# Kernel optimization log

Measured on AMD Instinct MI355X. Metric: run time of the kernel, lower is better.

Reference implementation:

```python
import jax, jax.numpy as jnp
import numpy as np

QLEN, MLEN, CMLEN, BSZ, D_MODEL = 1024, 1024, 512, 2, 1024
N_HEAD, D_HEAD, D_INNER = 16, 64, 4096
KLEN = MLEN + CMLEN + QLEN
LN_EPS = 1e-5


def _layer_norm(x, scale, bias):
    mu = jnp.mean(x, axis=-1, keepdims=True)
    var = jnp.var(x, axis=-1, keepdims=True)
    return (x - mu) * jax.lax.rsqrt(var + LN_EPS) * scale + bias


def _rel_shift(x):
    # x: [qlen, klen, bsz, n_head]  (Transformer-XL relative shift)
    q, k, b, n = x.shape
    x = jnp.concatenate([jnp.zeros((q, 1, b, n), x.dtype), x], axis=1)
    x = x.reshape(k + 1, q, b, n)[1:]
    return x.reshape(q, k, b, n)


def setup_inputs() -> dict:
    key = jax.random.key(0)
    ks = jax.random.split(key, 10)
    s = 0.02
    # causal mask: query i (absolute pos MLEN_TOT+i) cannot attend to key j > MLEN_TOT+i
    mlen_tot = KLEN - QLEN
    i = jnp.arange(QLEN)[:, None]
    j = jnp.arange(KLEN)[None, :]
    attn_mask = j > (i + mlen_tot)
    return {
        "input_ids": jax.random.normal(ks[0], (QLEN, BSZ, D_MODEL), jnp.float32),
        "pos_emb": jax.random.normal(ks[1], (KLEN, D_MODEL), jnp.float32),
        "mem": jax.random.normal(ks[2], (MLEN, BSZ, D_MODEL), jnp.float32),
        "c_mem": jax.random.normal(ks[3], (CMLEN, BSZ, D_MODEL), jnp.float32),
        "attn_mask": attn_mask,
        "qkv_w": jax.random.normal(ks[4], (D_MODEL, 3 * N_HEAD * D_HEAD), jnp.float32) * s,
        "r_w": jax.random.normal(ks[5], (D_MODEL, N_HEAD * D_HEAD), jnp.float32) * s,
        "o_w": jax.random.normal(ks[6], (N_HEAD * D_HEAD, D_MODEL), jnp.float32) * s,
        "r_w_bias": jax.random.normal(ks[7], (N_HEAD, D_HEAD), jnp.float32) * s,
        "r_r_bias": jax.random.normal(ks[8], (N_HEAD, D_HEAD), jnp.float32) * s,
        "ln_attn_scale": jnp.ones((D_MODEL,), jnp.float32),
        "ln_attn_bias": jnp.zeros((D_MODEL,), jnp.float32),
        "ff_w1": jax.random.normal(ks[9], (D_MODEL, D_INNER), jnp.float32) * s,
        "ff_b1": jnp.zeros((D_INNER,), jnp.float32),
        "ff_w2": jax.random.normal(jax.random.fold_in(key, 11), (D_INNER, D_MODEL), jnp.float32) * s,
        "ff_b2": jnp.zeros((D_MODEL,), jnp.float32),
        "ln_ff_scale": jnp.ones((D_MODEL,), jnp.float32),
        "ln_ff_bias": jnp.zeros((D_MODEL,), jnp.float32),
    }


def reference(input_ids, pos_emb, mem, c_mem, attn_mask, qkv_w, r_w, o_w,
              r_w_bias, r_r_bias, ln_attn_scale, ln_attn_bias,
              ff_w1, ff_b1, ff_w2, ff_b2, ln_ff_scale, ln_ff_bias):
    qlen, bsz, d_model = input_ids.shape
    n_head, d_head = r_w_bias.shape
    scale = 1.0 / np.sqrt(d_head)

    # _concat_memories + cat with current sequence (seq-first, dim 0)
    mems = jnp.concatenate([mem, c_mem], axis=0)
    cat = jnp.concatenate([mems, input_ids], axis=0)          # [klen, b, d]

    w_heads = cat @ qkv_w                                     # [klen, b, 3*h*dh]
    w_q, w_k, w_v = jnp.split(w_heads, 3, axis=-1)
    w_q = w_q[-qlen:]
    klen = w_k.shape[0]

    w_q = w_q.reshape(qlen, bsz, n_head, d_head)
    w_k = w_k.reshape(klen, bsz, n_head, d_head)
    w_v = w_v.reshape(klen, bsz, n_head, d_head)
    r_k = (pos_emb @ r_w).reshape(klen, n_head, d_head)       # [klen, h, dh]

    AC = jnp.einsum('ibnd,jbnd->ijbn', w_q + r_w_bias, w_k)
    BD = jnp.einsum('ibnd,jnd->ijbn', w_q + r_r_bias, r_k)
    BD = _rel_shift(BD)
    attn_score = (AC + BD) * scale                            # [q, k, b, h]

    attn_score = jnp.where(attn_mask[:, :, None, None], jnp.float32(-1e30), attn_score)
    attn_prob = jax.nn.softmax(attn_score, axis=1)

    attn_vec = jnp.einsum('ijbn,jbnd->ibnd', attn_prob, w_v)
    attn_vec = attn_vec.reshape(qlen, bsz, n_head * d_head)
    attn_out = attn_vec @ o_w

    # post-lnorm residual (pre_lnorm=False)
    attn_res = _layer_norm(input_ids + attn_out, ln_attn_scale, ln_attn_bias)

    # PositionwiseFF (post-lnorm)
    h = jax.nn.relu(attn_res @ ff_w1 + ff_b1) @ ff_w2 + ff_b2
    out = _layer_norm(attn_res + h, ln_ff_scale, ln_ff_bias)
    return out
```

## Files before the change

kernel.cpp:

```cpp
#include <hip/hip_runtime.h>
#include <hip/hip_bf16.h>

#define QLEN 1024
#define KLEN 2560
#define MTOT 1536
#define BSZ 2
#define NH 16
#define DH 64
#define DMODEL 1024
#define DINNER 4096

typedef short bf16x8 __attribute__((ext_vector_type(8)));
typedef float f32x4  __attribute__((ext_vector_type(4)));

__device__ __forceinline__ short f2bf(float f) {
    union { float f; unsigned u; } v; v.f = f;
    unsigned r = v.u + 0x7FFFu + ((v.u >> 16) & 1u);
    return (short)(r >> 16);
}
__device__ __forceinline__ float bf2f(short s) {
    union { unsigned u; float f; } v; v.u = ((unsigned)(unsigned short)s) << 16;
    return v.f;
}
__device__ __forceinline__ unsigned pack2(float a, float b) {
    return (unsigned)(unsigned short)f2bf(a) | ((unsigned)(unsigned short)f2bf(b) << 16);
}

#define GLOAD16(g, l)                                                        \
    __builtin_amdgcn_global_load_lds(                                        \
        (const __attribute__((address_space(1))) unsigned int*)(g),          \
        (__attribute__((address_space(3))) unsigned int*)(l), 16, 0, 0)

__device__ __forceinline__ void tr_body(
    const float* __restrict__ in, short* __restrict__ out,
    int K, int N, int bx, int by, int tid, float (*ts)[65])
{
    const int k0 = by * 64, n0 = bx * 64;
    const int r = tid >> 2, cb = (tid & 3) * 16;
    #pragma unroll
    for (int u = 0; u < 16; u += 4) {
        const float4 v = *(const float4*)(in + (size_t)(k0 + r) * N + n0 + cb + u);
        ts[r][cb + u] = v.x; ts[r][cb + u + 1] = v.y;
        ts[r][cb + u + 2] = v.z; ts[r][cb + u + 3] = v.w;
    }
    __syncthreads();
    #pragma unroll
    for (int p = 0; p < 4; p++) {
        const int wr_ = (tid >> 4) + p * 16;
        const int c   = (tid & 15) * 4;
        uint2 pk;
        pk.x = pack2(ts[c][wr_], ts[c + 1][wr_]);
        pk.y = pack2(ts[c + 2][wr_], ts[c + 3][wr_]);
        *(uint2*)(out + (size_t)(n0 + wr_) * K + k0 + c) = pk;
    }
}

__global__ __launch_bounds__(256) void prep_all(
    const float* __restrict__ mem, const float* __restrict__ cmem,
    const float* __restrict__ inp, short* __restrict__ catb,
    const float* __restrict__ pos, short* __restrict__ posb,
    const float* __restrict__ qkv_w, short* __restrict__ qkv_wt,
    const float* __restrict__ r_w, short* __restrict__ r_wt,
    const float* __restrict__ o_w, short* __restrict__ o_wt,
    const float* __restrict__ ff_w1, short* __restrict__ ff1t,
    const float* __restrict__ ff_w2, short* __restrict__ ff2t)
{
    __shared__ float ts[64][65];
    const int bid = blockIdx.x;
    const int tid = threadIdx.x;
    if (bid < 2560) {
        const int i = bid * 256 + tid;
        const int row = i >> 7, c = (i & 127) * 8;
        const float* src;
        if (row < 2048)      src = mem  + (size_t)row * 1024;
        else if (row < 3072) src = cmem + (size_t)(row - 2048) * 1024;
        else                 src = inp  + (size_t)(row - 3072) * 1024;
        const float4 a = *(const float4*)(src + c);
        const float4 b = *(const float4*)(src + c + 4);
        uint4 o;
        o.x = pack2(a.x, a.y); o.y = pack2(a.z, a.w);
        o.z = pack2(b.x, b.y); o.w = pack2(b.z, b.w);
        *(uint4*)(catb + (size_t)i * 8) = o;
    } else if (bid < 3840) {
        const int i = (bid - 2560) * 256 + tid;
        const float4 a = *(const float4*)(pos + (size_t)i * 8);
        const float4 b = *(const float4*)(pos + (size_t)i * 8 + 4);
        uint4 o;
        o.x = pack2(a.x, a.y); o.y = pack2(a.z, a.w);
        o.z = pack2(b.x, b.y); o.w = pack2(b.z, b.w);
        *(uint4*)(posb + (size_t)i * 8) = o;
    } else if (bid < 4608) {
        const int r = bid - 3840; tr_body(qkv_w, qkv_wt, 1024, 3072, r % 48, r / 48, tid, ts);
    } else if (bid < 4864) {
        const int r = bid - 4608; tr_body(r_w, r_wt, 1024, 1024, r % 16, r / 16, tid, ts);
    } else if (bid < 5120) {
        const int r = bid - 4864; tr_body(o_w, o_wt, 1024, 1024, r % 16, r / 16, tid, ts);
    } else if (bid < 6144) {
        const int r = bid - 5120; tr_body(ff_w1, ff1t, 1024, 4096, r % 64, r / 64, tid, ts);
    } else {
        const int r = bid - 6144; tr_body(ff_w2, ff2t, 4096, 1024, r % 16, r / 16, tid, ts);
    }
}

__global__ __launch_bounds__(256) void vt_conv(
    const short* __restrict__ wh, short* __restrict__ vt)
{
    __shared__ short Ts[64][72];
    const int j0 = blockIdx.x * 64;
    const int bn = blockIdx.y;
    const int b = bn >> 4, n = bn & 15;
    const int tid = threadIdx.x;
    {
        const int key = tid >> 2, c = (tid & 3) * 16;
        const short* p = wh + ((size_t)(j0 + key) * BSZ + b) * 3072 + 2048 + n * 64 + c;
        *(bf16x8*)&Ts[key][c]     = *(const bf16x8*)p;
        *(bf16x8*)&Ts[key][c + 8] = *(const bf16x8*)(p + 8);
    }
    __syncthreads();
    {
        const int d = tid >> 2, kc = (tid & 3) * 16;
        __attribute__((aligned(16))) short tmp[16];
        #pragma unroll
        for (int u = 0; u < 16; u++) tmp[u] = Ts[kc + u][d];
        short* q = vt + ((size_t)(bn * 64) + d) * KLEN + j0 + kc;
        *(uint4*)q       = *(uint4*)tmp;
        *(uint4*)(q + 8) = *((uint4*)tmp + 1);
    }
}

__device__ __forceinline__ void gemm_core(
    const short* __restrict__ A, const short* __restrict__ Bt,
    short* As, short* Bs, int Kfull, int klen, int bm, int bn,
    int tid, f32x4 acc[4][4])
{
    const int w  = tid >> 6;
    const int l  = tid & 63;
    const int lg = l >> 4, lc = l & 15;
    const int wr = w >> 1, wc = w & 1;
    const int srow = 2 * w * 16 + (l >> 2);
    const int scol = (l & 3) * 8;
    const size_t aoff0 = (size_t)(bm + srow) * Kfull + scol;
    const size_t boff0 = (size_t)(bn + srow) * Kfull + scol;
    const size_t rstep = (size_t)16 * Kfull;
    short* lA0 = As + 2 * w * 512;
    short* lA1 = As + (2 * w + 1) * 512;
    short* lB0 = Bs + 2 * w * 512;
    short* lB1 = Bs + (2 * w + 1) * 512;

    for (int k0 = 0; k0 < klen; k0 += 32) {
        GLOAD16(A + aoff0 + k0, lA0);
        GLOAD16(A + aoff0 + rstep + k0, lA1);
        GLOAD16(Bt + boff0 + k0, lB0);
        GLOAD16(Bt + boff0 + rstep + k0, lB1);
        __syncthreads();
        bf16x8 af[4], bfr[4];
        #pragma unroll
        for (int m = 0; m < 4; m++)
            af[m] = *(const bf16x8*)(As + (wr * 64 + m * 16 + lc) * 32 + lg * 8);
        #pragma unroll
        for (int n = 0; n < 4; n++)
            bfr[n] = *(const bf16x8*)(Bs + (wc * 64 + n * 16 + lc) * 32 + lg * 8);
        #pragma unroll
        for (int m = 0; m < 4; m++)
            #pragma unroll
            for (int n = 0; n < 4; n++)
                acc[m][n] = __builtin_amdgcn_mfma_f32_16x16x32_bf16(
                    af[m], bfr[n], acc[m][n], 0, 0, 0);
        __syncthreads();
    }
}

__global__ __launch_bounds__(256) void gemm_g12(
    const short* __restrict__ catb, const short* __restrict__ qkv_wt,
    short* __restrict__ whb,
    const short* __restrict__ posb, const short* __restrict__ r_wt,
    short* __restrict__ rkb)
{
    __shared__ short As[4096], Bs[4096];
    const int tid = threadIdx.x;
    int id = blockIdx.x;
    const short *A, *Bt; short* Cb; int N, bm, bn;
    if (id < 960) { A = catb; Bt = qkv_wt; Cb = whb; N = 3072;
                    bm = (id / 24) * 128; bn = (id % 24) * 128; }
    else { id -= 960; A = posb; Bt = r_wt; Cb = rkb; N = 1024;
           bm = (id / 8) * 128; bn = (id % 8) * 128; }

    f32x4 acc[4][4];
    #pragma unroll
    for (int m = 0; m < 4; m++)
        #pragma unroll
        for (int n = 0; n < 4; n++) acc[m][n] = (f32x4){0.f, 0.f, 0.f, 0.f};
    gemm_core(A, Bt, As, Bs, 1024, 1024, bm, bn, tid, acc);

    const int w = tid >> 6, l = tid & 63, lg = l >> 4, lc = l & 15;
    const int wr = w >> 1, wc = w & 1;
    #pragma unroll
    for (int m = 0; m < 4; m++)
        #pragma unroll
        for (int n = 0; n < 4; n++) {
            const int col = bn + wc * 64 + n * 16 + lc;
            #pragma unroll
            for (int r = 0; r < 4; r++) {
                const int row = bm + wr * 64 + m * 16 + lg * 4 + r;
                Cb[(size_t)row * N + col] = f2bf(acc[m][n][r]);
            }
        }
}

__global__ __launch_bounds__(256) void gemm_relu(
    const short* __restrict__ A, const short* __restrict__ Bt,
    const float* __restrict__ bias, short* __restrict__ Cb,
    int N, int K)
{
    __shared__ short As[4096], Bs[4096];
    const int tid = threadIdx.x;
    const int bm = blockIdx.y * 128, bn = blockIdx.x * 128;
    f32x4 acc[4][4];
    #pragma unroll
    for (int m = 0; m < 4; m++)
        #pragma unroll
        for (int n = 0; n < 4; n++) acc[m][n] = (f32x4){0.f, 0.f, 0.f, 0.f};
    gemm_core(A, Bt, As, Bs, K, K, bm, bn, tid, acc);

    const int w = tid >> 6, l = tid & 63, lg = l >> 4, lc = l & 15;
    const int wr = w >> 1, wc = w & 1;
    #pragma unroll
    for (int m = 0; m < 4; m++)
        #pragma unroll
        for (int n = 0; n < 4; n++) {
            const int col = bn + wc * 64 + n * 16 + lc;
            const float bv = bias[col];
            #pragma unroll
            for (int r = 0; r < 4; r++) {
                const int row = bm + wr * 64 + m * 16 + lg * 4 + r;
                Cb[(size_t)row * N + col] = f2bf(fmaxf(acc[m][n][r] + bv, 0.0f));
            }
        }
}

__global__ __launch_bounds__(256) void gemm_split(
    const short* __restrict__ A, const short* __restrict__ Bt,
    float* __restrict__ C0, float* __restrict__ C1,
    int N, int Kfull, int Ksub)
{
    __shared__ short As[4096], Bs[4096];
    const int tid = threadIdx.x;
    const int z = blockIdx.z;
    const int bm = blockIdx.y * 128, bn = blockIdx.x * 128;
    float* C = z ? C1 : C0;
    f32x4 acc[4][4];
    #pragma unroll
    for (int m = 0; m < 4; m++)
        #pragma unroll
        for (int n = 0; n < 4; n++) acc[m][n] = (f32x4){0.f, 0.f, 0.f, 0.f};
    gemm_core(A + z * Ksub, Bt + z * Ksub, As, Bs, Kfull, Ksub, bm, bn, tid, acc);

    const int w = tid >> 6, l = tid & 63, lg = l >> 4, lc = l & 15;
    const int wr = w >> 1, wc = w & 1;
    #pragma unroll
    for (int m = 0; m < 4; m++)
        #pragma unroll
        for (int n = 0; n < 4; n++) {
            const int col = bn + wc * 64 + n * 16 + lc;
            #pragma unroll
            for (int r = 0; r < 4; r++) {
                const int row = bm + wr * 64 + m * 16 + lg * 4 + r;
                C[(size_t)row * N + col] = acc[m][n][r];
            }
        }
}

__global__ __launch_bounds__(256) void attn_mfma(
    const short* __restrict__ wh,
    const short* __restrict__ vt,
    const short* __restrict__ rk,
    const float* __restrict__ rwb,
    const float* __restrict__ rrb,
    short* __restrict__ po,
    float* __restrict__ ml)
{
    __shared__ __align__(16) short Ks[64 * 64];
    __shared__ __align__(16) short Vs[64 * 64];
    __shared__ __align__(16) short Rs[128 * 64];
    __shared__ __align__(16) short Ps[4][16 * 64];

    const int bid = blockIdx.x;
    const int ib  = (bid >> 3) & 15;
    const int z   = (bid >> 7) & 1;
    const int bn  = ((bid & 7) << 2) | (bid >> 8);
    const int i0  = ib * 64;
    const int b   = bn >> 4, n = bn & 15;
    const int tid = threadIdx.x;
    const int w   = tid >> 6;
    const int l   = tid & 63;
    const int lg  = l >> 4;
    const int lc  = l & 15;
    const int i_base = i0 + 16 * w;

    bf16x8 aqw[2], aqr[2];
    {
        const int i = i_base + lc;
        const short* qp = wh + ((size_t)(MTOT + i) * BSZ + b) * 3072 + n * 64;
        #pragma unroll
        for (int kc = 0; kc < 2; kc++) {
            const bf16x8 q8 = *(const bf16x8*)(qp + kc * 32 + lg * 8);
            const int d0 = kc * 32 + lg * 8;
            #pragma unroll
            for (int e = 0; e < 8; e++) {
                const float qv = bf2f(q8[e]);
                aqw[kc][e] = f2bf(qv + rwb[n * 64 + d0 + e]);
                aqr[kc][e] = f2bf(qv + rrb[n * 64 + d0 + e]);
            }
        }
    }

    f32x4 o_acc[4];
    #pragma unroll
    for (int nt = 0; nt < 4; nt++) o_acc[nt] = (f32x4){0.f, 0.f, 0.f, 0.f};
    float mrun[4]  = {0.f, 0.f, 0.f, 0.f};
    float lpart[4] = {0.f, 0.f, 0.f, 0.f};

    const int jend   = i0 + 1600;
    const int jhalf  = (((jend >> 1) + 63) >> 6) << 6;
    const int jstart = z ? jhalf : 0;
    const int jstop  = z ? jend  : jhalf;

    const int kr0 = (tid * 2) >> 3,     kc0 = (tid * 2) & 7;
    const int kr1 = (tid * 2 + 1) >> 3, kc1 = (tid * 2 + 1) & 7;
    const size_t whK = (size_t)b * 3072 + 1024 + n * 64;
    const size_t vtK = (size_t)(bn * 64) * KLEN;

    bf16x8 pk0, pk1, pv0, pv1;
    pk0 = *(const bf16x8*)(wh + (size_t)(jstart + kr0) * BSZ * 3072 + whK + kc0 * 8);
    pk1 = *(const bf16x8*)(wh + (size_t)(jstart + kr1) * BSZ * 3072 + whK + kc1 * 8);
    pv0 = *(const bf16x8*)(vt + vtK + (size_t)kr0 * KLEN + jstart + kc0 * 8);
    pv1 = *(const bf16x8*)(vt + vtK + (size_t)kr1 * KLEN + jstart + kc1 * 8);

    for (int j0 = jstart; j0 < jstop; j0 += 64) {
        __syncthreads();
        bf16x8 rreg[4];
        const int mbase = j0 - i0 + 960;
        #pragma unroll
        for (int u = 0; u < 4; u++) {
            const int ci  = tid + 256 * u;
            const int row = ci >> 3, c = ci & 7;
            const int m   = mbase + row;
            rreg[u] = (m < KLEN)
                ? *(const bf16x8*)(rk + (size_t)m * 1024 + n * 64 + c * 8)
                : (bf16x8){0, 0, 0, 0, 0, 0, 0, 0};
        }
        *(bf16x8*)(Ks + kr0 * 64 + ((kc0 ^ (kr0 & 7)) * 8)) = pk0;
        *(bf16x8*)(Ks + kr1 * 64 + ((kc1 ^ (kr1 & 7)) * 8)) = pk1;
        *(bf16x8*)(Vs + kr0 * 64 + ((kc0 ^ (kr0 & 7)) * 8)) = pv0;
        *(bf16x8*)(Vs + kr1 * 64 + ((kc1 ^ (kr1 & 7)) * 8)) = pv1;
        #pragma unroll
        for (int u = 0; u < 4; u++) {
            const int ci  = tid + 256 * u;
            const int row = ci >> 3, c = ci & 7;
            *(bf16x8*)(Rs + row * 64 + ((c ^ (row & 7)) * 8)) = rreg[u];
        }
        const int jn = j0 + 64;
        if (jn < jstop) {
            pk0 = *(const bf16x8*)(wh + (size_t)(jn + kr0) * BSZ * 3072 + whK + kc0 * 8);
            pk1 = *(const bf16x8*)(wh + (size_t)(jn + kr1) * BSZ * 3072 + whK + kc1 * 8);
            pv0 = *(const bf16x8*)(vt + vtK + (size_t)kr0 * KLEN + jn + kc0 * 8);
            pv1 = *(const bf16x8*)(vt + vtK + (size_t)kr1 * KLEN + jn + kc1 * 8);
        }
        __syncthreads();

        __builtin_amdgcn_s_setprio(1);
        f32x4 sfr[4];
        #pragma unroll
        for (int jt = 0; jt < 4; jt++) {
            const int row = 16 * jt + lc;
            const int c0 = (lg ^ (row & 7)) * 8, c1 = ((4 + lg) ^ (row & 7)) * 8;
            const bf16x8 bk0 = *(const bf16x8*)(Ks + row * 64 + c0);
            const bf16x8 bk1 = *(const bf16x8*)(Ks + row * 64 + c1);
            f32x4 acc = (f32x4){0.f, 0.f, 0.f, 0.f};
            acc = __builtin_amdgcn_mfma_f32_16x16x32_bf16(aqw[0], bk0, acc, 0, 0, 0);
            acc = __builtin_amdgcn_mfma_f32_16x16x32_bf16(aqw[1], bk1, acc, 0, 0, 0);
            sfr[jt] = acc;
        }
        f32x4 dr[5];
        #pragma unroll
        for (int mt = 0; mt < 5; mt++) {
            const int rrow = 16 * mt + lc + 48 - 16 * w;
            const int c0 = (lg ^ (rrow & 7)) * 8, c1 = ((4 + lg) ^ (rrow & 7)) * 8;
            const bf16x8 br0 = *(const bf16x8*)(Rs + rrow * 64 + c0);
            const bf16x8 br1 = *(const bf16x8*)(Rs + rrow * 64 + c1);
            f32x4 acc = (f32x4){0.f, 0.f, 0.f, 0.f};
            acc = __builtin_amdgcn_mfma_f32_16x16x32_bf16(aqr[0], br0, acc, 0, 0, 0);
            acc = __builtin_amdgcn_mfma_f32_16x16x32_bf16(aqr[1], br1, acc, 0, 0, 0);
            dr[mt] = acc;
        }
        __builtin_amdgcn_s_setprio(0);

        #pragma unroll
        for (int r = 0; r < 4; r++) {
            const int q   = 4 * lg + r;
            const int o   = lc + 15 - q;
            const int src = (l & 48) | (o & 15);
            float sv[4];
            float mx = -1e30f;
            #pragma unroll
            for (int jt = 0; jt < 4; jt++) {
                const float v0 = __shfl(dr[jt][r], src);
                const float v1 = __shfl(dr[jt + 1][r], src);
                const float bd = (o < 16) ? v0 : v1;
                float s = (sfr[jt][r] + bd) * 0.125f;
                if (z) {
                    const int j = j0 + 16 * jt + lc;
                    if (j > i_base + q + MTOT) s = -1e30f;
                }
                sv[jt] = s;
                mx = fmaxf(mx, s);
            }
            if (__any(mx - mrun[r] > 8.0f)) {
                #pragma unroll
                for (int msk = 1; msk <= 8; msk <<= 1)
                    mx = fmaxf(mx, __shfl_xor(mx, msk));
                const float mnew = fmaxf(mrun[r], mx);
                const float corr = __expf(mrun[r] - mnew);
                mrun[r] = mnew;
                lpart[r] *= corr;
                #pragma unroll
                for (int nt = 0; nt < 4; nt++) o_acc[nt][r] *= corr;
            }
            float ps = 0.f;
            #pragma unroll
            for (int jt = 0; jt < 4; jt++) {
                const float p = __expf(sv[jt] - mrun[r]);
                ps += p;
                Ps[w][q * 64 + (((2 * jt + (lc >> 3)) ^ (q & 7)) * 8) + (lc & 7)] = f2bf(p);
            }
            lpart[r] += ps;
        }

        asm volatile("s_waitcnt lgkmcnt(0)" ::: "memory");
        __builtin_amdgcn_sched_barrier(0);

        __builtin_amdgcn_s_setprio(1);
        const int pc0 = (lg ^ (lc & 7)) * 8, pc1 = ((4 + lg) ^ (lc & 7)) * 8;
        const bf16x8 pa0 = *(const bf16x8*)(Ps[w] + lc * 64 + pc0);
        const bf16x8 pa1 = *(const bf16x8*)(Ps[w] + lc * 64 + pc1);
        #pragma unroll
        for (int nt = 0; nt < 4; nt++) {
            const int row = 16 * nt + lc;
            const int c0 = (lg ^ (row & 7)) * 8, c1 = ((4 + lg) ^ (row & 7)) * 8;
            const bf16x8 bv0 = *(const bf16x8*)(Vs + row * 64 + c0);
            const bf16x8 bv1 = *(const bf16x8*)(Vs + row * 64 + c1);
            o_acc[nt] = __builtin_amdgcn_mfma_f32_16x16x32_bf16(pa0, bv0, o_acc[nt], 0, 0, 0);
            o_acc[nt] = __builtin_amdgcn_mfma_f32_16x16x32_bf16(pa1, bv1, o_acc[nt], 0, 0, 0);
        }
        __builtin_amdgcn_s_setprio(0);
    }

    const size_t blk = (size_t)z * 512 + ib * 32 + bn;
    #pragma unroll
    for (int r = 0; r < 4; r++) {
        float lr = lpart[r];
        #pragma unroll
        for (int msk = 1; msk <= 8; msk <<= 1)
            lr += __shfl_xor(lr, msk);
        const int q = 16 * w + 4 * lg + r;
        #pragma unroll
        for (int nt = 0; nt < 4; nt++)
            po[(blk * 64 + q) * 64 + 16 * nt + lc] = f2bf(o_acc[nt][r]);
        if (lc == 0) {
            ml[(blk * 64 + q) * 2 + 0] = mrun[r];
            ml[(blk * 64 + q) * 2 + 1] = lr;
        }
    }
}

__global__ __launch_bounds__(256) void attn_merge(
    const short* __restrict__ po, const float* __restrict__ ml,
    short* __restrict__ av)
{
    const int blk = blockIdx.x;
    const int ib = blk >> 5, bn = blk & 31;
    const int b = bn >> 4, n = bn & 15;
    const int tid = threadIdx.x;
    const int q = tid >> 2, dc = (tid & 3) * 16;
    const size_t r0 = (size_t)blk * 64 + q;
    const size_t r1 = (size_t)(512 + blk) * 64 + q;
    const float m0 = ml[r0 * 2], l0 = ml[r0 * 2 + 1];
    const float m1 = ml[r1 * 2], l1 = ml[r1 * 2 + 1];
    const float M = fmaxf(m0, m1);
    const float c0 = __expf(m0 - M), c1 = __expf(m1 - M);
    const float invL = 1.0f / (l0 * c0 + l1 * c1);
    const bf16x8 a0 = *(const bf16x8*)(po + r0 * 64 + dc);
    const bf16x8 a1 = *(const bf16x8*)(po + r0 * 64 + dc + 8);
    const bf16x8 b0 = *(const bf16x8*)(po + r1 * 64 + dc);
    const bf16x8 b1 = *(const bf16x8*)(po + r1 * 64 + dc + 8);
    __attribute__((aligned(16))) short ov[16];
    #pragma unroll
    for (int e = 0; e < 8; e++) {
        ov[e]     = f2bf((bf2f(a0[e]) * c0 + bf2f(b0[e]) * c1) * invL);
        ov[e + 8] = f2bf((bf2f(a1[e]) * c0 + bf2f(b1[e]) * c1) * invL);
    }
    const int i = ib * 64 + q;
    short* op = av + ((size_t)i * BSZ + b) * 1024 + n * 64 + dc;
    *(uint4*)op       = *(uint4*)ov;
    *(uint4*)(op + 8) = *((uint4*)ov + 1);
}

template <bool WB, bool HASB>
__global__ __launch_bounds__(256) void ln_fuse(
    const float* __restrict__ p0, const float* __restrict__ p1,
    const float* __restrict__ badd, const float* __restrict__ res,
    const float* __restrict__ scale, const float* __restrict__ bias,
    float* __restrict__ out, short* __restrict__ outb)
{
    const int row = blockIdx.x;
    const int tid = threadIdx.x;
    const size_t base = (size_t)row * 1024 + tid * 4;
    const float4 a = *(const float4*)(p0 + base);
    const float4 b = *(const float4*)(p1 + base);
    const float4 rv = *(const float4*)(res + base);
    float v[4] = {a.x + b.x + rv.x, a.y + b.y + rv.y,
                  a.z + b.z + rv.z, a.w + b.w + rv.w};
    if (HASB) {
        const float4 bb = *(const float4*)(badd + tid * 4);
        v[0] += bb.x; v[1] += bb.y; v[2] += bb.z; v[3] += bb.w;
    }
    float s  = v[0] + v[1] + v[2] + v[3];
    float ss = v[0]*v[0] + v[1]*v[1] + v[2]*v[2] + v[3]*v[3];
    #pragma unroll
    for (int off = 32; off >= 1; off >>= 1) {
        s  += __shfl_down(s, off);
        ss += __shfl_down(ss, off);
    }
    __shared__ float red[8];
    const int lane = tid & 63, wid = tid >> 6;
    if (lane == 0) { red[wid] = s; red[4 + wid] = ss; }
    __syncthreads();
    if (tid == 0) {
        red[0] = red[0] + red[1] + red[2] + red[3];
        red[4] = red[4] + red[5] + red[6] + red[7];
    }
    __syncthreads();
    const float mean = red[0] * (1.0f / 1024.0f);
    const float var  = red[4] * (1.0f / 1024.0f) - mean * mean;
    const float rstd = rsqrtf(var + 1e-5f);
    const float4 sc = *(const float4*)(scale + tid * 4);
    const float4 bi = *(const float4*)(bias + tid * 4);
    float4 o;
    o.x = (v[0] - mean) * rstd * sc.x + bi.x;
    o.y = (v[1] - mean) * rstd * sc.y + bi.y;
    o.z = (v[2] - mean) * rstd * sc.z + bi.z;
    o.w = (v[3] - mean) * rstd * sc.w + bi.w;
    *(float4*)(out + base) = o;
    if (WB) {
        uint2 pk;
        pk.x = pack2(o.x, o.y);
        pk.y = pack2(o.z, o.w);
        *(uint2*)(outb + base) = pk;
    }
}

extern "C" void kernel_launch(void* const* d_in, const int* in_sizes, int n_in,
                              void* d_out, int out_size, void* d_ws, size_t ws_size,
                              hipStream_t stream) {
    const float* input_ids = (const float*)d_in[0];
    const float* pos_emb   = (const float*)d_in[1];
    const float* mem       = (const float*)d_in[2];
    const float* c_mem     = (const float*)d_in[3];
    const float* qkv_w     = (const float*)d_in[5];
    const float* r_w       = (const float*)d_in[6];
    const float* o_w       = (const float*)d_in[7];
    const float* r_w_bias  = (const float*)d_in[8];
    const float* r_r_bias  = (const float*)d_in[9];
    const float* ln_a_s    = (const float*)d_in[10];
    const float* ln_a_b    = (const float*)d_in[11];
    const float* ff_w1     = (const float*)d_in[12];
    const float* ff_b1     = (const float*)d_in[13];
    const float* ff_w2     = (const float*)d_in[14];
    const float* ff_b2     = (const float*)d_in[15];
    const float* ln_f_s    = (const float*)d_in[16];
    const float* ln_f_b    = (const float*)d_in[17];

    char* base = (char*)d_ws;
    short* o_wt   = (short*)(base + 0);
    short* ff1t   = (short*)(base + 2097152);
    short* ff2t   = (short*)(base + 10485760);
    short* whb    = (short*)(base + 18874368);
    short* rkb    = (short*)(base + 50331648);
    short* qkv_wt = (short*)(base + 55574528);
    short* catb   = (short*)(base + 61865984);
    short* posb   = (short*)(base + 72351744);
    short* r_wt   = (short*)(base + 77594624);
    short* vtb    = (short*)(base + 55574528);
    short* po     = (short*)(base + 66060288);
    float* mlb    = (float*)(base + 74448896);
    short* avb    = (short*)(base + 74973184);
    float* hp0    = (float*)(base + 18874368);
    float* hp1    = (float*)(base + 27262976);
    float* ares   = (float*)(base + 35651584);
    short* aresb  = (short*)(base + 44040192);
    short* h1b    = (short*)(base + 48234496);

    const dim3 thr(256);

    prep_all<<<dim3(7168), thr, 0, stream>>>(
        mem, c_mem, input_ids, catb, pos_emb, posb,
        qkv_w, qkv_wt, r_w, r_wt, o_w, o_wt, ff_w1, ff1t, ff_w2, ff2t);
    gemm_g12<<<dim3(1120), thr, 0, stream>>>(catb, qkv_wt, whb, posb, r_wt, rkb);
    vt_conv<<<dim3(40, 32), thr, 0, stream>>>(whb, vtb);
    attn_mfma<<<dim3(1024), thr, 0, stream>>>(
        whb, vtb, rkb, r_w_bias, r_r_bias, po, mlb);
    attn_merge<<<dim3(512), thr, 0, stream>>>(po, mlb, avb);
    gemm_split<<<dim3(8, 16, 2), thr, 0, stream>>>(
        avb, o_wt, hp0, hp1, 1024, 1024, 512);
    ln_fuse<true, false><<<dim3(2048), thr, 0, stream>>>(
        hp0, hp1, nullptr, input_ids, ln_a_s, ln_a_b, ares, aresb);
    gemm_relu<<<dim3(32, 16), thr, 0, stream>>>(aresb, ff1t, ff_b1, h1b, 4096, 1024);
    gemm_split<<<dim3(8, 16, 2), thr, 0, stream>>>(
        h1b, ff2t, hp0, hp1, 1024, 4096, 2048);
    ln_fuse<false, true><<<dim3(2048), thr, 0, stream>>>(
        hp0, hp1, ff_b2, ares, ln_f_s, ln_f_b, (float*)d_out, nullptr);
}
```

Before: 295.0 us.

## Widen attention blocks to 128 queries with 8 waves sharing K/V tiles

The attention kernel now uses 512-thread blocks covering 128 query rows instead of 64, so each K, V and positional tile loaded into shared memory serves twice as many queries. Grid size halves, each thread loads one K/V chunk and three R rows, and the R window grows to 192 rows. The merge kernel's indexing is updated to match the new partial-output layout. This cuts global and LDS traffic per query at the cost of fewer blocks, coarser causal-split balance and more shared memory per block.

New measurement: 403.3 us. +36.7%, slower.

```diff
diff --git a/kernel.cpp b/kernel.cpp
--- a/kernel.cpp
+++ b/kernel.cpp
@@ -270,7 +270,7 @@
         }
 }
 
-__global__ __launch_bounds__(256) void attn_mfma(
+__global__ __launch_bounds__(512, 4) void attn_mfma(
     const short* __restrict__ wh,
     const short* __restrict__ vt,
     const short* __restrict__ rk,
@@ -281,14 +281,14 @@
 {
     __shared__ __align__(16) short Ks[64 * 64];
     __shared__ __align__(16) short Vs[64 * 64];
-    __shared__ __align__(16) short Rs[128 * 64];
-    __shared__ __align__(16) short Ps[4][16 * 64];
+    __shared__ __align__(16) short Rs[192 * 64];
+    __shared__ __align__(16) short Ps[8][16 * 64];
 
     const int bid = blockIdx.x;
-    const int ib  = (bid >> 3) & 15;
-    const int z   = (bid >> 7) & 1;
-    const int bn  = ((bid & 7) << 2) | (bid >> 8);
-    const int i0  = ib * 64;
+    const int ibp = (bid >> 3) & 7;
+    const int z   = (bid >> 6) & 1;
+    const int bn  = ((bid & 7) << 2) | (bid >> 7);
+    const int i0  = ibp * 128;
     const int b   = bn >> 4, n = bn & 15;
     const int tid = threadIdx.x;
     const int w   = tid >> 6;
@@ -320,51 +320,41 @@
     float mrun[4]  = {0.f, 0.f, 0.f, 0.f};
     float lpart[4] = {0.f, 0.f, 0.f, 0.f};
 
-    const int jend   = i0 + 1600;
-    const int jhalf  = (((jend >> 1) + 63) >> 6) << 6;
+    const int jend   = i0 + 1664;
+    const int jhalf  = i0 / 2 + 832;
     const int jstart = z ? jhalf : 0;
     const int jstop  = z ? jend  : jhalf;
 
-    const int kr0 = (tid * 2) >> 3,     kc0 = (tid * 2) & 7;
-    const int kr1 = (tid * 2 + 1) >> 3, kc1 = (tid * 2 + 1) & 7;
+    const int kr = tid >> 3, kc = tid & 7;
     const size_t whK = (size_t)b * 3072 + 1024 + n * 64;
     const size_t vtK = (size_t)(bn * 64) * KLEN;
 
-    bf16x8 pk0, pk1, pv0, pv1;
-    pk0 = *(const bf16x8*)(wh + (size_t)(jstart + kr0) * BSZ * 3072 + whK + kc0 * 8);
-    pk1 = *(const bf16x8*)(wh + (size_t)(jstart + kr1) * BSZ * 3072 + whK + kc1 * 8);
-    pv0 = *(const bf16x8*)(vt + vtK + (size_t)kr0 * KLEN + jstart + kc0 * 8);
-    pv1 = *(const bf16x8*)(vt + vtK + (size_t)kr1 * KLEN + jstart + kc1 * 8);
+    bf16x8 pk, pv;
+    pk = *(const bf16x8*)(wh + (size_t)(jstart + kr) * (BSZ * 3072) + whK + kc * 8);
+    pv = *(const bf16x8*)(vt + vtK + (size_t)kr * KLEN + jstart + kc * 8);
 
     for (int j0 = jstart; j0 < jstop; j0 += 64) {
         __syncthreads();
-        bf16x8 rreg[4];
-        const int mbase = j0 - i0 + 960;
-        #pragma unroll
-        for (int u = 0; u < 4; u++) {
-            const int ci  = tid + 256 * u;
-            const int row = ci >> 3, c = ci & 7;
-            const int m   = mbase + row;
+        bf16x8 rreg[3];
+        const int mbase = j0 - i0 + 896;
+        #pragma unroll
+        for (int u = 0; u < 3; u++) {
+            const int m = mbase + kr + 64 * u;
             rreg[u] = (m < KLEN)
-                ? *(const bf16x8*)(rk + (size_t)m * 1024 + n * 64 + c * 8)
+                ? *(const bf16x8*)(rk + (size_t)m * 1024 + n * 64 + kc * 8)
                 : (bf16x8){0, 0, 0, 0, 0, 0, 0, 0};
         }
-        *(bf16x8*)(Ks + kr0 * 64 + ((kc0 ^ (kr0 & 7)) * 8)) = pk0;
-        *(bf16x8*)(Ks + kr1 * 64 + ((kc1 ^ (kr1 & 7)) * 8)) = pk1;
-        *(bf16x8*)(Vs + kr0 * 64 + ((kc0 ^ (kr0 & 7)) * 8)) = pv0;
-        *(bf16x8*)(Vs + kr1 * 64 + ((kc1 ^ (kr1 & 7)) * 8)) = pv1;
-        #pragma unroll
-        for (int u = 0; u < 4; u++) {
-            const int ci  = tid + 256 * u;
-            const int row = ci >> 3, c = ci & 7;
-            *(bf16x8*)(Rs + row * 64 + ((c ^ (row & 7)) * 8)) = rreg[u];
+        *(bf16x8*)(Ks + kr * 64 + ((kc ^ (kr & 7)) * 8)) = pk;
+        *(bf16x8*)(Vs + kr * 64 + ((kc ^ (kr & 7)) * 8)) = pv;
+        #pragma unroll
+        for (int u = 0; u < 3; u++) {
+            const int row = kr + 64 * u;
+            *(bf16x8*)(Rs + row * 64 + ((kc ^ (row & 7)) * 8)) = rreg[u];
         }
         const int jn = j0 + 64;
         if (jn < jstop) {
-            pk0 = *(const bf16x8*)(wh + (size_t)(jn + kr0) * BSZ * 3072 + whK + kc0 * 8);
-            pk1 = *(const bf16x8*)(wh + (size_t)(jn + kr1) * BSZ * 3072 + whK + kc1 * 8);
-            pv0 = *(const bf16x8*)(vt + vtK + (size_t)kr0 * KLEN + jn + kc0 * 8);
-            pv1 = *(const bf16x8*)(vt + vtK + (size_t)kr1 * KLEN + jn + kc1 * 8);
+            pk = *(const bf16x8*)(wh + (size_t)(jn + kr) * (BSZ * 3072) + whK + kc * 8);
+            pv = *(const bf16x8*)(vt + vtK + (size_t)kr * KLEN + jn + kc * 8);
         }
         __syncthreads();
 
@@ -384,7 +374,7 @@
         f32x4 dr[5];
         #pragma unroll
         for (int mt = 0; mt < 5; mt++) {
-            const int rrow = 16 * mt + lc + 48 - 16 * w;
+            const int rrow = 16 * mt + lc + 112 - 16 * w;
             const int c0 = (lg ^ (rrow & 7)) * 8, c1 = ((4 + lg) ^ (rrow & 7)) * 8;
             const bf16x8 br0 = *(const bf16x8*)(Rs + rrow * 64 + c0);
             const bf16x8 br1 = *(const bf16x8*)(Rs + rrow * 64 + c1);
@@ -455,7 +445,7 @@
         __builtin_amdgcn_s_setprio(0);
     }
 
-    const size_t blk = (size_t)z * 512 + ib * 32 + bn;
+    const size_t blk = (size_t)z * 256 + ibp * 32 + bn;
     #pragma unroll
     for (int r = 0; r < 4; r++) {
         float lr = lpart[r];
@@ -465,10 +455,10 @@
         const int q = 16 * w + 4 * lg + r;
         #pragma unroll
         for (int nt = 0; nt < 4; nt++)
-            po[(blk * 64 + q) * 64 + 16 * nt + lc] = f2bf(o_acc[nt][r]);
+            po[(blk * 128 + q) * 64 + 16 * nt + lc] = f2bf(o_acc[nt][r]);
         if (lc == 0) {
-            ml[(blk * 64 + q) * 2 + 0] = mrun[r];
-            ml[(blk * 64 + q) * 2 + 1] = lr;
+            ml[(blk * 128 + q) * 2 + 0] = mrun[r];
+            ml[(blk * 128 + q) * 2 + 1] = lr;
         }
     }
 }
@@ -478,12 +468,13 @@
     short* __restrict__ av)
 {
     const int blk = blockIdx.x;
-    const int ib = blk >> 5, bn = blk & 31;
+    const int ib2 = blk >> 5, bn = blk & 31;
     const int b = bn >> 4, n = bn & 15;
     const int tid = threadIdx.x;
-    const int q = tid >> 2, dc = (tid & 3) * 16;
-    const size_t r0 = (size_t)blk * 64 + q;
-    const size_t r1 = (size_t)(512 + blk) * 64 + q;
+    const int q64 = tid >> 2, dc = (tid & 3) * 16;
+    const int i = ib2 * 64 + q64;
+    const size_t r0 = ((size_t)(i >> 7) * 32 + bn) * 128 + (i & 127);
+    const size_t r1 = ((size_t)(256 + (i >> 7) * 32 + bn)) * 128 + (i & 127);
     const float m0 = ml[r0 * 2], l0 = ml[r0 * 2 + 1];
     const float m1 = ml[r1 * 2], l1 = ml[r1 * 2 + 1];
     const float M = fmaxf(m0, m1);
@@ -499,7 +490,6 @@
         ov[e]     = f2bf((bf2f(a0[e]) * c0 + bf2f(b0[e]) * c1) * invL);
         ov[e + 8] = f2bf((bf2f(a1[e]) * c0 + bf2f(b1[e]) * c1) * invL);
     }
-    const int i = ib * 64 + q;
     short* op = av + ((size_t)i * BSZ + b) * 1024 + n * 64 + dc;
     *(uint4*)op       = *(uint4*)ov;
     *(uint4*)(op + 8) = *((uint4*)ov + 1);
@@ -607,7 +597,7 @@
         qkv_w, qkv_wt, r_w, r_wt, o_w, o_wt, ff_w1, ff1t, ff_w2, ff2t);
     gemm_g12<<<dim3(1120), thr, 0, stream>>>(catb, qkv_wt, whb, posb, r_wt, rkb);
     vt_conv<<<dim3(40, 32), thr, 0, stream>>>(whb, vtb);
-    attn_mfma<<<dim3(1024), thr, 0, stream>>>(
+    attn_mfma<<<dim3(512), dim3(512), 0, stream>>>(
         whb, vtb, rkb, r_w_bias, r_r_bias, po, mlb);
     attn_merge<<<dim3(512), thr, 0, stream>>>(po, mlb, avb);
     gemm_split<<<dim3(8, 16, 2), thr, 0, stream>>>(
```
